# Performance work log

Hardware: AMD Instinct MI355X
Metric: run time of the kernel (lower is better)

The kernel has to match this reference:

```python
import jax, jax.numpy as jnp
import numpy as np

HEADS = 2
HID = 128
IN_DIM = 128
OUT_DIM = 1
N_NODES = 50000
NEG_SLOPE = 0.2  # PyG GATConv default
EPS = 1e-16


def setup_inputs() -> dict:
    key = jax.random.key(0)
    ks = jax.random.split(key, 16)
    N, E = N_NODES, 800000
    x = jax.random.normal(ks[0], (N, IN_DIM), dtype=jnp.float32)
    edge_index = jax.random.randint(ks[1], (2, E), 0, N, dtype=jnp.int32)
    s = 0.1
    # GATConv 1: in=128 -> heads=2, out=128 per head
    W1 = jax.random.normal(ks[2], (IN_DIM, HEADS * HID), dtype=jnp.float32) * s
    a_src1 = jax.random.normal(ks[3], (HEADS, HID), dtype=jnp.float32) * s
    a_dst1 = jax.random.normal(ks[4], (HEADS, HID), dtype=jnp.float32) * s
    b1 = jnp.zeros((HEADS * HID,), dtype=jnp.float32)
    # GATConv 2: in=256 -> heads=2, out=128 per head
    W2 = jax.random.normal(ks[5], (HEADS * HID, HEADS * HID), dtype=jnp.float32) * s
    a_src2 = jax.random.normal(ks[6], (HEADS, HID), dtype=jnp.float32) * s
    a_dst2 = jax.random.normal(ks[7], (HEADS, HID), dtype=jnp.float32) * s
    b2 = jnp.zeros((HEADS * HID,), dtype=jnp.float32)
    # post_mp: Linear(256,128) -> Dropout -> Linear(128,1)
    Wp1 = jax.random.normal(ks[8], (HEADS * HID, HID), dtype=jnp.float32) * s
    bp1 = jnp.zeros((HID,), dtype=jnp.float32)
    Wp2 = jax.random.normal(ks[9], (HID, OUT_DIM), dtype=jnp.float32) * s
    bp2 = jnp.zeros((OUT_DIM,), dtype=jnp.float32)
    return {"x": x, "edge_index": edge_index,
            "W1": W1, "a_src1": a_src1, "a_dst1": a_dst1, "b1": b1,
            "W2": W2, "a_src2": a_src2, "a_dst2": a_dst2, "b2": b2,
            "Wp1": Wp1, "bp1": bp1, "Wp2": Wp2, "bp2": bp2}


def gat_conv(x, src, dst, W, a_src, a_dst, b, num_nodes):
    """PyG-style GATConv (concat=True). src/dst already include self-loops."""
    N = num_nodes
    h = (x @ W).reshape(N, HEADS, HID)                        # [N,H,C]
    alpha_s = jnp.einsum('nhc,hc->nh', h, a_src)              # [N,H]
    alpha_d = jnp.einsum('nhc,hc->nh', h, a_dst)              # [N,H]
    e = jax.nn.leaky_relu(alpha_s[src] + alpha_d[dst], NEG_SLOPE)  # [E,H]
    # segment softmax over destination node
    emax = jax.ops.segment_max(e, dst, num_segments=N)        # [N,H]
    emax = jnp.where(jnp.isfinite(emax), emax, 0.0)
    w = jnp.exp(e - emax[dst])                                # [E,H]
    denom = jax.ops.segment_sum(w, dst, num_segments=N)       # [N,H]
    alpha = w / (denom[dst] + EPS)                            # [E,H]
    out = jax.ops.segment_sum(h[src] * alpha[:, :, None], dst, num_segments=N)
    return out.reshape(N, HEADS * HID) + b


def reference(x, edge_index, W1, a_src1, a_dst1, b1, W2, a_src2, a_dst2, b2,
              Wp1, bp1, Wp2, bp2):
    N = x.shape[0]
    loops = jnp.arange(N, dtype=edge_index.dtype)
    src = jnp.concatenate([edge_index[0], loops])
    dst = jnp.concatenate([edge_index[1], loops])
    h = gat_conv(x, src, dst, W1, a_src1, a_dst1, b1, N)
    h = jax.nn.relu(h)  # dropout is identity in eval mode
    h = gat_conv(h, src, dst, W2, a_src2, a_dst2, b2, N)
    h = jax.nn.relu(h)
    h = h @ Wp1 + bp1
    h = h @ Wp2 + bp2
    return jax.nn.sigmoid(h)
```

## Files before the change

### kernel.cpp

```cpp
#include <hip/hip_runtime.h>

#define HID 128
#define C2 256
#define NEG 0.2f

typedef __bf16 v8bf __attribute__((ext_vector_type(8)));
typedef float  v4f  __attribute__((ext_vector_type(4)));
typedef float  v2f  __attribute__((ext_vector_type(2)));
typedef unsigned short us8 __attribute__((ext_vector_type(8)));

__device__ __forceinline__ float bf2f(unsigned short u) {
    union { float f; unsigned int i; } v; v.i = ((unsigned int)u) << 16; return v.f;
}
__device__ __forceinline__ unsigned short f2bf(float f) {
    union { float f; unsigned int i; } v; v.f = f;
    unsigned int r = v.i + 0x7FFFu + ((v.i >> 16) & 1u);
    return (unsigned short)(r >> 16);
}
__device__ __forceinline__ unsigned char f2fp8(float f) {
    return (unsigned char)(__builtin_amdgcn_cvt_pk_fp8_f32(f, f, 0, false) & 0xFF);
}
__device__ __forceinline__ float lrelu(float x) { return x > 0.f ? x : NEG * x; }

__global__ __launch_bounds__(256) void packB(const float* __restrict__ W,
                                             unsigned short* __restrict__ out,
                                             int K, int N) {
    int idx = blockIdx.x * 256 + threadIdx.x;
    int ksteps = K >> 5;
    int total = (N >> 4) * ksteps * 64;
    if (idx >= total) return;
    int lane = idx & 63;
    int rest = idx >> 6;
    int nt = rest / ksteps, k0 = rest - nt * ksteps;
    int n = nt * 16 + (lane & 15);
    int kb = k0 * 32 + (lane >> 4) * 8;
    us8 v;
#pragma unroll
    for (int j = 0; j < 8; ++j) v[j] = f2bf(W[(size_t)(kb + j) * N + n]);
    *(us8*)(out + (size_t)idx * 8) = v;
}

__global__ void zero_int(int* p, int n) {
    int i = blockIdx.x * 256 + threadIdx.x;
    if (i < n) p[i] = 0;
}

__global__ void hist_rank_kernel(const int* __restrict__ ei, int* __restrict__ cnt,
                                 int* __restrict__ rank, int E) {
    int i = blockIdx.x * 256 + threadIdx.x;
    if (i >= E) return;
    int d = ei[E + i];
    rank[i] = atomicAdd(&cnt[d], 1);
}

__global__ __launch_bounds__(256) void scanA(const int* __restrict__ cnt, int* __restrict__ rs,
                                             int* __restrict__ part, int N) {
    __shared__ int s[256];
    int t = threadIdx.x, i = blockIdx.x * 256 + t;
    int v = (i < N) ? cnt[i] : 0;
    s[t] = v; __syncthreads();
    for (int off = 1; off < 256; off <<= 1) {
        int x = (t >= off) ? s[t - off] : 0;
        __syncthreads();
        s[t] += x;
        __syncthreads();
    }
    if (i < N) rs[i] = s[t] - v;
    if (t == 255) part[blockIdx.x] = s[255];
}

__global__ __launch_bounds__(256) void scanB(int* __restrict__ part, int n) {
    __shared__ int s[256];
    int t = threadIdx.x;
    int v = (t < n) ? part[t] : 0;
    s[t] = v; __syncthreads();
    for (int off = 1; off < 256; off <<= 1) {
        int x = (t >= off) ? s[t - off] : 0;
        __syncthreads();
        s[t] += x;
        __syncthreads();
    }
    if (t < n) part[t] = s[t] - v;
}

__global__ void scanC(int* __restrict__ rs, const int* __restrict__ part, int N, int E) {
    int i = blockIdx.x * 256 + threadIdx.x;
    if (i < N) rs[i] += part[blockIdx.x];
    if (i == 0) rs[N] = E;
}

__global__ void scatter_kernel(const int* __restrict__ ei, const int* __restrict__ rs,
                               const int* __restrict__ rank, int* __restrict__ csr, int E) {
    int i = blockIdx.x * 256 + threadIdx.x;
    if (i >= E) return;
    int s = ei[i], d = ei[E + i];
    csr[rs[d] + rank[i]] = s;
}

template<bool AFP32, int G>
__global__ __launch_bounds__(256) void gemm_alpha(const void* __restrict__ Av,
                                                  const unsigned short* __restrict__ Bp,
                                                  const float* __restrict__ asrc,
                                                  const float* __restrict__ adst,
                                                  float* __restrict__ asd,
                                                  unsigned char* __restrict__ C,
                                                  int M, int N, int K) {
    int ksteps = K >> 5;
    int ngrp = N >> 7;
    int mtiles = M >> 4;
    int groups = (mtiles + G - 1) / G;
    int w = (blockIdx.x << 2) + (threadIdx.x >> 6);
    int mp = w / ngrp, g = w - mp * ngrp;
    if (mp >= groups) return;
    int lane = threadIdx.x & 63;
    int l16 = lane & 15, quad = lane >> 4;

    int mrow[G];
#pragma unroll
    for (int gi = 0; gi < G; ++gi) {
        int mt = mp * G + gi;
        mrow[gi] = (mt < mtiles ? mt : mtiles - 1) * 16 + l16;
    }

    const unsigned short* Bf = Bp + ((size_t)(g * 8) * ksteps << 9) + lane * 8;
    v4f acc[G][8];
#pragma unroll
    for (int gi = 0; gi < G; ++gi)
#pragma unroll
        for (int t = 0; t < 8; ++t) acc[gi][t] = (v4f){0, 0, 0, 0};

    for (int k0 = 0; k0 < ksteps; ++k0) {
        v8bf a[G];
        if (AFP32) {
            const float* A = (const float*)Av;
#pragma unroll
            for (int gi = 0; gi < G; ++gi) {
                const float* p = A + (size_t)mrow[gi] * K + k0 * 32 + quad * 8;
                float4 u0 = *(const float4*)p, u1 = *(const float4*)(p + 4);
                a[gi][0]=(__bf16)u0.x; a[gi][1]=(__bf16)u0.y; a[gi][2]=(__bf16)u0.z; a[gi][3]=(__bf16)u0.w;
                a[gi][4]=(__bf16)u1.x; a[gi][5]=(__bf16)u1.y; a[gi][6]=(__bf16)u1.z; a[gi][7]=(__bf16)u1.w;
            }
        } else {
            const unsigned short* A = (const unsigned short*)Av;
#pragma unroll
            for (int gi = 0; gi < G; ++gi)
                a[gi] = *(const v8bf*)(A + (size_t)mrow[gi] * K + k0 * 32 + quad * 8);
        }
#pragma unroll
        for (int t = 0; t < 8; ++t) {
            v8bf bfr = *(const v8bf*)(Bf + ((size_t)(t * ksteps + k0) << 9));
#pragma unroll
            for (int gi = 0; gi < G; ++gi)
                acc[gi][t] = __builtin_amdgcn_mfma_f32_16x16x32_bf16(a[gi], bfr, acc[gi][t], 0, 0, 0);
        }
    }

    int n0 = g << 7;
    float sv[8], dv[8];
#pragma unroll
    for (int t = 0; t < 8; ++t) {
        int col = n0 + t * 16 + l16;
        sv[t] = asrc[col];
        dv[t] = adst[col];
    }
#pragma unroll
    for (int gi = 0; gi < G; ++gi) {
        int mt = mp * G + gi;
        if (mt >= mtiles) break;
        int row0 = mt * 16 + quad * 4;
#pragma unroll
        for (int r = 0; r < 4; ++r) {
            float sa = 0.f, sd = 0.f;
#pragma unroll
            for (int t = 0; t < 8; ++t) {
                int col = n0 + t * 16 + l16;
                float hv = acc[gi][t][r];
                C[(size_t)(row0 + r) * N + col] = f2fp8(hv);
                sa += hv * sv[t];
                sd += hv * dv[t];
            }
#pragma unroll
            for (int off = 8; off; off >>= 1) {
                sa += __shfl_xor(sa, off);
                sd += __shfl_xor(sd, off);
            }
            if (l16 == 0) {
                int row = row0 + r;
                asd[(size_t)row * 4 + g]     = sa;
                asd[(size_t)row * 4 + 2 + g] = sd;
            }
        }
    }
}

__global__ __launch_bounds__(256) void agg_kernel(const int* __restrict__ rs,
                                                  const int* __restrict__ csr,
                                                  const unsigned char* __restrict__ h,
                                                  const float* __restrict__ asd,
                                                  const float* __restrict__ bias,
                                                  unsigned short* __restrict__ out, int N) {
    int d = blockIdx.x * 4 + (threadIdx.x >> 6);
    if (d >= N) return;
    int lane = threadIdx.x & 63;
    int beg = rs[d], end = rs[d + 1];
    int e2 = lane >> 5;
    int sub = lane & 31;
    int head = sub >> 4;
    float adh = asd[(size_t)d * 4 + 2 + head];
    int cbase = sub * 8;
    const unsigned char* hc = h + cbase;
    float a[8];
#pragma unroll
    for (int j = 0; j < 8; ++j) a[j] = 0.f;
    float den = 0.f;
#pragma unroll 2
    for (int i = beg; i < end; i += 2) {
        int ei = i + e2;
        bool valid = ei < end;
        int s = csr[valid ? ei : end - 1];
        float e = lrelu(asd[(size_t)s * 4 + head] + adh);
        float wgt = valid ? __expf(e) : 0.f;
        den += wgt;
        uint2 u = *(const uint2*)(hc + (size_t)s * C2);
        v2f p0 = __builtin_amdgcn_cvt_pk_f32_fp8(u.x, false);
        v2f p1 = __builtin_amdgcn_cvt_pk_f32_fp8(u.x, true);
        v2f p2 = __builtin_amdgcn_cvt_pk_f32_fp8(u.y, false);
        v2f p3 = __builtin_amdgcn_cvt_pk_f32_fp8(u.y, true);
        a[0] += wgt * p0.x; a[1] += wgt * p0.y;
        a[2] += wgt * p1.x; a[3] += wgt * p1.y;
        a[4] += wgt * p2.x; a[5] += wgt * p2.y;
        a[6] += wgt * p3.x; a[7] += wgt * p3.y;
    }
#pragma unroll
    for (int j = 0; j < 8; ++j) a[j] += __shfl_xor(a[j], 32);
    den += __shfl_xor(den, 32);
    if (e2 == 0) {
        float wS = __expf(lrelu(asd[(size_t)d * 4 + head] + adh));
        uint2 u = *(const uint2*)(hc + (size_t)d * C2);
        v2f p0 = __builtin_amdgcn_cvt_pk_f32_fp8(u.x, false);
        v2f p1 = __builtin_amdgcn_cvt_pk_f32_fp8(u.x, true);
        v2f p2 = __builtin_amdgcn_cvt_pk_f32_fp8(u.y, false);
        v2f p3 = __builtin_amdgcn_cvt_pk_f32_fp8(u.y, true);
        a[0] += wS * p0.x; a[1] += wS * p0.y;
        a[2] += wS * p1.x; a[3] += wS * p1.y;
        a[4] += wS * p2.x; a[5] += wS * p2.y;
        a[6] += wS * p3.x; a[7] += wS * p3.y;
        float rden = 1.f / (den + wS + 1e-16f);
        us8 o;
#pragma unroll
        for (int j = 0; j < 8; ++j) o[j] = f2bf(fmaxf(a[j] * rden + bias[cbase + j], 0.f));
        *(us8*)(out + (size_t)d * C2 + cbase) = o;
    }
}

template<int G>
__global__ __launch_bounds__(256) void gemm_final(const unsigned short* __restrict__ A,
                                                  const unsigned short* __restrict__ Bp,
                                                  const float* __restrict__ bp1,
                                                  const float* __restrict__ wp2,
                                                  const float* __restrict__ bp2,
                                                  float* __restrict__ out,
                                                  int M, int K) {
    int ksteps = K >> 5;
    int mtiles = M >> 4;
    int groups = (mtiles + G - 1) / G;
    int mp = (blockIdx.x << 2) + (threadIdx.x >> 6);
    if (mp >= groups) return;
    int lane = threadIdx.x & 63;
    int l16 = lane & 15, quad = lane >> 4;

    int mrow[G];
#pragma unroll
    for (int gi = 0; gi < G; ++gi) {
        int mt = mp * G + gi;
        mrow[gi] = (mt < mtiles ? mt : mtiles - 1) * 16 + l16;
    }

    const unsigned short* Bf = Bp + lane * 8;
    v4f acc[G][8];
#pragma unroll
    for (int gi = 0; gi < G; ++gi)
#pragma unroll
        for (int t = 0; t < 8; ++t) acc[gi][t] = (v4f){0, 0, 0, 0};
    for (int k0 = 0; k0 < ksteps; ++k0) {
        v8bf a[G];
#pragma unroll
        for (int gi = 0; gi < G; ++gi)
            a[gi] = *(const v8bf*)(A + (size_t)mrow[gi] * K + k0 * 32 + quad * 8);
#pragma unroll
        for (int t = 0; t < 8; ++t) {
            v8bf bfr = *(const v8bf*)(Bf + ((size_t)(t * ksteps + k0) << 9));
#pragma unroll
            for (int gi = 0; gi < G; ++gi)
                acc[gi][t] = __builtin_amdgcn_mfma_f32_16x16x32_bf16(a[gi], bfr, acc[gi][t], 0, 0, 0);
        }
    }
    float wv[8], bv[8];
#pragma unroll
    for (int t = 0; t < 8; ++t) {
        int col = t * 16 + l16;
        wv[t] = wp2[col];
        bv[t] = bp1[col];
    }
    float bias2 = bp2[0];
#pragma unroll
    for (int gi = 0; gi < G; ++gi) {
        int mt = mp * G + gi;
        if (mt >= mtiles) break;
        int row0 = mt * 16 + quad * 4;
#pragma unroll
        for (int r = 0; r < 4; ++r) {
            float s = 0.f;
#pragma unroll
            for (int t = 0; t < 8; ++t) s += (acc[gi][t][r] + bv[t]) * wv[t];
#pragma unroll
            for (int off = 8; off; off >>= 1) s += __shfl_xor(s, off);
            if (l16 == 0) {
                float xv = s + bias2;
                out[row0 + r] = 1.f / (1.f + __expf(-xv));
            }
        }
    }
}

extern "C" void kernel_launch(void* const* d_in, const int* in_sizes, int n_in,
                              void* d_out, int out_size, void* d_ws, size_t ws_size,
                              hipStream_t stream) {
    const float* x   = (const float*)d_in[0];
    const int*   ei  = (const int*)d_in[1];
    const float* W1  = (const float*)d_in[2];
    const float* as1 = (const float*)d_in[3];
    const float* ad1 = (const float*)d_in[4];
    const float* b1  = (const float*)d_in[5];
    const float* W2  = (const float*)d_in[6];
    const float* as2 = (const float*)d_in[7];
    const float* ad2 = (const float*)d_in[8];
    const float* b2  = (const float*)d_in[9];
    const float* Wp1 = (const float*)d_in[10];
    const float* bp1 = (const float*)d_in[11];
    const float* Wp2 = (const float*)d_in[12];
    const float* bp2 = (const float*)d_in[13];
    float* out = (float*)d_out;

    int NN = in_sizes[0] / HID;
    int E  = in_sizes[1] / 2;

    char* ws = (char*)d_ws;
    size_t off = 0;
    auto alloc = [&](size_t bytes) -> char* {
        char* p = ws + off;
        off += (bytes + 255) & ~(size_t)255;
        return p;
    };
    unsigned char*  bufH = (unsigned char*)alloc((size_t)NN * C2);
    unsigned short* bufO = (unsigned short*)alloc((size_t)NN * C2 * 2);
    float* asd = (float*)alloc((size_t)NN * 4 * sizeof(float));
    int* rs    = (int*)alloc((size_t)(NN + 1) * 4);
    int* cnt   = (int*)alloc((size_t)NN * 4);
    int* rank  = (int*)alloc((size_t)E * 4);
    int* csr   = (int*)alloc((size_t)E * 4);
    int* part  = (int*)alloc(1024);
    unsigned short* W1p  = (unsigned short*)alloc((size_t)HID * C2 * 2);
    unsigned short* W2p  = (unsigned short*)alloc((size_t)C2 * C2 * 2);
    unsigned short* Wp1p = (unsigned short*)alloc((size_t)C2 * HID * 2);

    int nchunk = (NN + 255) / 256;
    int eblk   = (E + 255) / 256;

    packB<<<(HID * C2 / 8 + 255) / 256, 256, 0, stream>>>(W1, W1p, HID, C2);
    packB<<<(C2 * C2 / 8 + 255) / 256, 256, 0, stream>>>(W2, W2p, C2, C2);
    packB<<<(C2 * HID / 8 + 255) / 256, 256, 0, stream>>>(Wp1, Wp1p, C2, HID);

    zero_int<<<nchunk, 256, 0, stream>>>(cnt, NN);
    hist_rank_kernel<<<eblk, 256, 0, stream>>>(ei, cnt, rank, E);
    scanA<<<nchunk, 256, 0, stream>>>(cnt, rs, part, NN);
    scanB<<<1, 256, 0, stream>>>(part, nchunk);
    scanC<<<nchunk, 256, 0, stream>>>(rs, part, NN, E);
    scatter_kernel<<<eblk, 256, 0, stream>>>(ei, rs, rank, csr, E);

    const int G = 2;
    int mtiles = NN / 16;
    int groups = (mtiles + G - 1) / G;
    int wgemm = groups * 2;
    int aggGrid = (NN + 3) / 4;

    gemm_alpha<true, G><<<(wgemm + 3) / 4, 256, 0, stream>>>(x, W1p, as1, ad1, asd, bufH, NN, C2, HID);
    agg_kernel<<<aggGrid, 256, 0, stream>>>(rs, csr, bufH, asd, b1, bufO, NN);
    gemm_alpha<false, G><<<(wgemm + 3) / 4, 256, 0, stream>>>(bufO, W2p, as2, ad2, asd, bufH, NN, C2, C2);
    agg_kernel<<<aggGrid, 256, 0, stream>>>(rs, csr, bufH, asd, b2, bufO, NN);
    gemm_final<G><<<(groups + 3) / 4, 256, 0, stream>>>(bufO, Wp1p, bp1, Wp2, bp2, out, NN, C2);
}
```

Measured before the change: 299.0 us.

## Stage B tiles in LDS shared across waves in GEMMs, pack agg FMAs, memset counts

```diff
diff --git a/kernel.cpp b/kernel.cpp
--- a/kernel.cpp
+++ b/kernel.cpp
@@ -40,11 +40,6 @@
     *(us8*)(out + (size_t)idx * 8) = v;
 }
 
-__global__ void zero_int(int* p, int n) {
-    int i = blockIdx.x * 256 + threadIdx.x;
-    if (i < n) p[i] = 0;
-}
-
 __global__ void hist_rank_kernel(const int* __restrict__ ei, int* __restrict__ cnt,
                                  int* __restrict__ rank, int E) {
     int i = blockIdx.x * 256 + threadIdx.x;
@@ -105,53 +100,66 @@
                                                   float* __restrict__ asd,
                                                   unsigned char* __restrict__ C,
                                                   int M, int N, int K) {
+    const int kc = 4;
     int ksteps = K >> 5;
     int ngrp = N >> 7;
     int mtiles = M >> 4;
-    int groups = (mtiles + G - 1) / G;
-    int w = (blockIdx.x << 2) + (threadIdx.x >> 6);
-    int mp = w / ngrp, g = w - mp * ngrp;
-    if (mp >= groups) return;
-    int lane = threadIdx.x & 63;
+    int bm = 4 * G;
+    int g = blockIdx.x % ngrp, mblk = blockIdx.x / ngrp;
+    int wv = threadIdx.x >> 6, lane = threadIdx.x & 63;
     int l16 = lane & 15, quad = lane >> 4;
+    int mt0 = mblk * bm + wv * G;
+
+    __shared__ unsigned short Bs[8 * kc * 512];
 
     int mrow[G];
 #pragma unroll
     for (int gi = 0; gi < G; ++gi) {
-        int mt = mp * G + gi;
+        int mt = mt0 + gi;
         mrow[gi] = (mt < mtiles ? mt : mtiles - 1) * 16 + l16;
     }
 
-    const unsigned short* Bf = Bp + ((size_t)(g * 8) * ksteps << 9) + lane * 8;
+    const us8* srcB = (const us8*)Bp + (size_t)(g * 8) * ksteps * 64;
     v4f acc[G][8];
 #pragma unroll
     for (int gi = 0; gi < G; ++gi)
 #pragma unroll
         for (int t = 0; t < 8; ++t) acc[gi][t] = (v4f){0, 0, 0, 0};
 
-    for (int k0 = 0; k0 < ksteps; ++k0) {
-        v8bf a[G];
-        if (AFP32) {
-            const float* A = (const float*)Av;
-#pragma unroll
-            for (int gi = 0; gi < G; ++gi) {
-                const float* p = A + (size_t)mrow[gi] * K + k0 * 32 + quad * 8;
-                float4 u0 = *(const float4*)p, u1 = *(const float4*)(p + 4);
-                a[gi][0]=(__bf16)u0.x; a[gi][1]=(__bf16)u0.y; a[gi][2]=(__bf16)u0.z; a[gi][3]=(__bf16)u0.w;
-                a[gi][4]=(__bf16)u1.x; a[gi][5]=(__bf16)u1.y; a[gi][6]=(__bf16)u1.z; a[gi][7]=(__bf16)u1.w;
-            }
-        } else {
-            const unsigned short* A = (const unsigned short*)Av;
-#pragma unroll
-            for (int gi = 0; gi < G; ++gi)
-                a[gi] = *(const v8bf*)(A + (size_t)mrow[gi] * K + k0 * 32 + quad * 8);
-        }
-#pragma unroll
-        for (int t = 0; t < 8; ++t) {
-            v8bf bfr = *(const v8bf*)(Bf + ((size_t)(t * ksteps + k0) << 9));
-#pragma unroll
-            for (int gi = 0; gi < G; ++gi)
-                acc[gi][t] = __builtin_amdgcn_mfma_f32_16x16x32_bf16(a[gi], bfr, acc[gi][t], 0, 0, 0);
+    for (int c0 = 0; c0 < ksteps; c0 += kc) {
+        __syncthreads();
+        for (int f = threadIdx.x; f < 8 * kc * 64; f += 256) {
+            int t = f >> 8;
+            int rem = f & 255;
+            int kr = rem >> 6, l = rem & 63;
+            ((us8*)Bs)[f] = srcB[((size_t)t * ksteps + c0 + kr) * 64 + l];
+        }
+        __syncthreads();
+        for (int kr = 0; kr < kc; ++kr) {
+            int k0 = c0 + kr;
+            v8bf a[G];
+            if (AFP32) {
+                const float* A = (const float*)Av;
+#pragma unroll
+                for (int gi = 0; gi < G; ++gi) {
+                    const float* p = A + (size_t)mrow[gi] * K + k0 * 32 + quad * 8;
+                    float4 u0 = *(const float4*)p, u1 = *(const float4*)(p + 4);
+                    a[gi][0]=(__bf16)u0.x; a[gi][1]=(__bf16)u0.y; a[gi][2]=(__bf16)u0.z; a[gi][3]=(__bf16)u0.w;
+                    a[gi][4]=(__bf16)u1.x; a[gi][5]=(__bf16)u1.y; a[gi][6]=(__bf16)u1.z; a[gi][7]=(__bf16)u1.w;
+                }
+            } else {
+                const unsigned short* A = (const unsigned short*)Av;
+#pragma unroll
+                for (int gi = 0; gi < G; ++gi)
+                    a[gi] = *(const v8bf*)(A + (size_t)mrow[gi] * K + k0 * 32 + quad * 8);
+            }
+#pragma unroll
+            for (int t = 0; t < 8; ++t) {
+                v8bf bfr = ((const v8bf*)Bs)[(t * kc + kr) * 64 + lane];
+#pragma unroll
+                for (int gi = 0; gi < G; ++gi)
+                    acc[gi][t] = __builtin_amdgcn_mfma_f32_16x16x32_bf16(a[gi], bfr, acc[gi][t], 0, 0, 0);
+            }
         }
     }
 
@@ -165,7 +173,7 @@
     }
 #pragma unroll
     for (int gi = 0; gi < G; ++gi) {
-        int mt = mp * G + gi;
+        int mt = mt0 + gi;
         if (mt >= mtiles) break;
         int row0 = mt * 16 + quad * 4;
 #pragma unroll
@@ -209,9 +217,7 @@
     float adh = asd[(size_t)d * 4 + 2 + head];
     int cbase = sub * 8;
     const unsigned char* hc = h + cbase;
-    float a[8];
-#pragma unroll
-    for (int j = 0; j < 8; ++j) a[j] = 0.f;
+    v2f a01 = {0, 0}, a23 = {0, 0}, a45 = {0, 0}, a67 = {0, 0};
     float den = 0.f;
 #pragma unroll 2
     for (int i = beg; i < end; i += 2) {
@@ -222,15 +228,13 @@
         float wgt = valid ? __expf(e) : 0.f;
         den += wgt;
         uint2 u = *(const uint2*)(hc + (size_t)s * C2);
-        v2f p0 = __builtin_amdgcn_cvt_pk_f32_fp8(u.x, false);
-        v2f p1 = __builtin_amdgcn_cvt_pk_f32_fp8(u.x, true);
-        v2f p2 = __builtin_amdgcn_cvt_pk_f32_fp8(u.y, false);
-        v2f p3 = __builtin_amdgcn_cvt_pk_f32_fp8(u.y, true);
-        a[0] += wgt * p0.x; a[1] += wgt * p0.y;
-        a[2] += wgt * p1.x; a[3] += wgt * p1.y;
-        a[4] += wgt * p2.x; a[5] += wgt * p2.y;
-        a[6] += wgt * p3.x; a[7] += wgt * p3.y;
-    }
+        v2f w2 = {wgt, wgt};
+        a01 += w2 * __builtin_amdgcn_cvt_pk_f32_fp8(u.x, false);
+        a23 += w2 * __builtin_amdgcn_cvt_pk_f32_fp8(u.x, true);
+        a45 += w2 * __builtin_amdgcn_cvt_pk_f32_fp8(u.y, false);
+        a67 += w2 * __builtin_amdgcn_cvt_pk_f32_fp8(u.y, true);
+    }
+    float a[8] = {a01.x, a01.y, a23.x, a23.y, a45.x, a45.y, a67.x, a67.y};
 #pragma unroll
     for (int j = 0; j < 8; ++j) a[j] += __shfl_xor(a[j], 32);
     den += __shfl_xor(den, 32);
@@ -261,58 +265,73 @@
                                                   const float* __restrict__ bp2,
                                                   float* __restrict__ out,
                                                   int M, int K) {
+    const int kc = 4;
     int ksteps = K >> 5;
     int mtiles = M >> 4;
-    int groups = (mtiles + G - 1) / G;
-    int mp = (blockIdx.x << 2) + (threadIdx.x >> 6);
-    if (mp >= groups) return;
-    int lane = threadIdx.x & 63;
+    int bm = 4 * G;
+    int mblk = blockIdx.x;
+    int wv = threadIdx.x >> 6, lane = threadIdx.x & 63;
     int l16 = lane & 15, quad = lane >> 4;
+    int mt0 = mblk * bm + wv * G;
+
+    __shared__ unsigned short Bs[8 * kc * 512];
 
     int mrow[G];
 #pragma unroll
     for (int gi = 0; gi < G; ++gi) {
-        int mt = mp * G + gi;
+        int mt = mt0 + gi;
         mrow[gi] = (mt < mtiles ? mt : mtiles - 1) * 16 + l16;
     }
 
-    const unsigned short* Bf = Bp + lane * 8;
+    const us8* srcB = (const us8*)Bp;
     v4f acc[G][8];
 #pragma unroll
     for (int gi = 0; gi < G; ++gi)
 #pragma unroll
         for (int t = 0; t < 8; ++t) acc[gi][t] = (v4f){0, 0, 0, 0};
-    for (int k0 = 0; k0 < ksteps; ++k0) {
-        v8bf a[G];
-#pragma unroll
-        for (int gi = 0; gi < G; ++gi)
-            a[gi] = *(const v8bf*)(A + (size_t)mrow[gi] * K + k0 * 32 + quad * 8);
-#pragma unroll
-        for (int t = 0; t < 8; ++t) {
-            v8bf bfr = *(const v8bf*)(Bf + ((size_t)(t * ksteps + k0) << 9));
+
+    for (int c0 = 0; c0 < ksteps; c0 += kc) {
+        __syncthreads();
+        for (int f = threadIdx.x; f < 8 * kc * 64; f += 256) {
+            int t = f >> 8;
+            int rem = f & 255;
+            int kr = rem >> 6, l = rem & 63;
+            ((us8*)Bs)[f] = srcB[((size_t)t * ksteps + c0 + kr) * 64 + l];
+        }
+        __syncthreads();
+        for (int kr = 0; kr < kc; ++kr) {
+            int k0 = c0 + kr;
+            v8bf a[G];
 #pragma unroll
             for (int gi = 0; gi < G; ++gi)
-                acc[gi][t] = __builtin_amdgcn_mfma_f32_16x16x32_bf16(a[gi], bfr, acc[gi][t], 0, 0, 0);
-        }
-    }
-    float wv[8], bv[8];
+                a[gi] = *(const v8bf*)(A + (size_t)mrow[gi] * K + k0 * 32 + quad * 8);
+#pragma unroll
+            for (int t = 0; t < 8; ++t) {
+                v8bf bfr = ((const v8bf*)Bs)[(t * kc + kr) * 64 + lane];
+#pragma unroll
+                for (int gi = 0; gi < G; ++gi)
+                    acc[gi][t] = __builtin_amdgcn_mfma_f32_16x16x32_bf16(a[gi], bfr, acc[gi][t], 0, 0, 0);
+            }
+        }
+    }
+    float wv8[8], bv[8];
 #pragma unroll
     for (int t = 0; t < 8; ++t) {
         int col = t * 16 + l16;
-        wv[t] = wp2[col];
+        wv8[t] = wp2[col];
         bv[t] = bp1[col];
     }
     float bias2 = bp2[0];
 #pragma unroll
     for (int gi = 0; gi < G; ++gi) {
-        int mt = mp * G + gi;
+        int mt = mt0 + gi;
         if (mt >= mtiles) break;
         int row0 = mt * 16 + quad * 4;
 #pragma unroll
         for (int r = 0; r < 4; ++r) {
             float s = 0.f;
 #pragma unroll
-            for (int t = 0; t < 8; ++t) s += (acc[gi][t][r] + bv[t]) * wv[t];
+            for (int t = 0; t < 8; ++t) s += (acc[gi][t][r] + bv[t]) * wv8[t];
 #pragma unroll
             for (int off = 8; off; off >>= 1) s += __shfl_xor(s, off);
             if (l16 == 0) {
@@ -371,7 +390,7 @@
     packB<<<(C2 * C2 / 8 + 255) / 256, 256, 0, stream>>>(W2, W2p, C2, C2);
     packB<<<(C2 * HID / 8 + 255) / 256, 256, 0, stream>>>(Wp1, Wp1p, C2, HID);
 
-    zero_int<<<nchunk, 256, 0, stream>>>(cnt, NN);
+    hipMemsetAsync(cnt, 0, (size_t)NN * 4, stream);
     hist_rank_kernel<<<eblk, 256, 0, stream>>>(ei, cnt, rank, E);
     scanA<<<nchunk, 256, 0, stream>>>(cnt, rs, part, NN);
     scanB<<<1, 256, 0, stream>>>(part, nchunk);
@@ -380,13 +399,13 @@
 
     const int G = 2;
     int mtiles = NN / 16;
-    int groups = (mtiles + G - 1) / G;
-    int wgemm = groups * 2;
+    int bm = 4 * G;
+    int groups = (mtiles + bm - 1) / bm;
     int aggGrid = (NN + 3) / 4;
 
-    gemm_alpha<true, G><<<(wgemm + 3) / 4, 256, 0, stream>>>(x, W1p, as1, ad1, asd, bufH, NN, C2, HID);
+    gemm_alpha<true, G><<<groups * 2, 256, 0, stream>>>(x, W1p, as1, ad1, asd, bufH, NN, C2, HID);
     agg_kernel<<<aggGrid, 256, 0, stream>>>(rs, csr, bufH, asd, b1, bufO, NN);
-    gemm_alpha<false, G><<<(wgemm + 3) / 4, 256, 0, stream>>>(bufO, W2p, as2, ad2, asd, bufH, NN, C2, C2);
+    gemm_alpha<false, G><<<groups * 2, 256, 0, stream>>>(bufO, W2p, as2, ad2, asd, bufH, NN, C2, C2);
     agg_kernel<<<aggGrid, 256, 0, stream>>>(rs, csr, bufH, asd, b2, bufO, NN);
-    gemm_final<G><<<(groups + 3) / 4, 256, 0, stream>>>(bufO, Wp1p, bp1, Wp2, bp2, out, NN, C2);
-}
+    gemm_final<G><<<groups, 256, 0, stream>>>(bufO, Wp1p, bp1, Wp2, bp2, out, NN, C2);
+}
```

New measurement: 302.4 us. Within noise of the previous version (+1.1%).

## Fuse prep kernels, overlap CSR scatter with GEMM, and vectorize fp8 stores

Applied to the files above, without the earlier changes.

```diff
diff --git a/kernel.cpp b/kernel.cpp
--- a/kernel.cpp
+++ b/kernel.cpp
@@ -17,22 +17,18 @@
     unsigned int r = v.i + 0x7FFFu + ((v.i >> 16) & 1u);
     return (unsigned short)(r >> 16);
 }
-__device__ __forceinline__ unsigned char f2fp8(float f) {
-    return (unsigned char)(__builtin_amdgcn_cvt_pk_fp8_f32(f, f, 0, false) & 0xFF);
-}
 __device__ __forceinline__ float lrelu(float x) { return x > 0.f ? x : NEG * x; }
 
-__global__ __launch_bounds__(256) void packB(const float* __restrict__ W,
-                                             unsigned short* __restrict__ out,
-                                             int K, int N) {
-    int idx = blockIdx.x * 256 + threadIdx.x;
+__device__ __forceinline__ void packB_body(const float* __restrict__ W,
+                                           unsigned short* __restrict__ out,
+                                           int K, int N, int idx) {
     int ksteps = K >> 5;
     int total = (N >> 4) * ksteps * 64;
     if (idx >= total) return;
     int lane = idx & 63;
     int rest = idx >> 6;
-    int nt = rest / ksteps, k0 = rest - nt * ksteps;
-    int n = nt * 16 + (lane & 15);
+    int tt = rest / ksteps, k0 = rest - tt * ksteps;
+    int n = (tt >> 3) * 128 + (lane & 15) * 8 + (tt & 7);
     int kb = k0 * 32 + (lane >> 4) * 8;
     us8 v;
 #pragma unroll
@@ -40,14 +36,20 @@
     *(us8*)(out + (size_t)idx * 8) = v;
 }
 
-__global__ void zero_int(int* p, int n) {
-    int i = blockIdx.x * 256 + threadIdx.x;
-    if (i < n) p[i] = 0;
-}
-
-__global__ void hist_rank_kernel(const int* __restrict__ ei, int* __restrict__ cnt,
-                                 int* __restrict__ rank, int E) {
-    int i = blockIdx.x * 256 + threadIdx.x;
+__global__ __launch_bounds__(256) void prep_kernel(const float* __restrict__ W1, unsigned short* W1p,
+                                                   const float* __restrict__ W2, unsigned short* W2p,
+                                                   const float* __restrict__ Wp1, unsigned short* Wp1p,
+                                                   const int* __restrict__ ei, int* __restrict__ cnt,
+                                                   int* __restrict__ rank, int E,
+                                                   int b1, int b2, int b3) {
+    int b = blockIdx.x;
+    if (b < b1) { packB_body(W1, W1p, HID, C2, b * 256 + threadIdx.x); return; }
+    b -= b1;
+    if (b < b2) { packB_body(W2, W2p, C2, C2, b * 256 + threadIdx.x); return; }
+    b -= b2;
+    if (b < b3) { packB_body(Wp1, Wp1p, C2, HID, b * 256 + threadIdx.x); return; }
+    b -= b3;
+    int i = b * 256 + threadIdx.x;
     if (i >= E) return;
     int d = ei[E + i];
     rank[i] = atomicAdd(&cnt[d], 1);
@@ -89,14 +91,6 @@
     if (i == 0) rs[N] = E;
 }
 
-__global__ void scatter_kernel(const int* __restrict__ ei, const int* __restrict__ rs,
-                               const int* __restrict__ rank, int* __restrict__ csr, int E) {
-    int i = blockIdx.x * 256 + threadIdx.x;
-    if (i >= E) return;
-    int s = ei[i], d = ei[E + i];
-    csr[rs[d] + rank[i]] = s;
-}
-
 template<bool AFP32, int G>
 __global__ __launch_bounds__(256) void gemm_alpha(const void* __restrict__ Av,
                                                   const unsigned short* __restrict__ Bp,
@@ -104,21 +98,34 @@
                                                   const float* __restrict__ adst,
                                                   float* __restrict__ asd,
                                                   unsigned char* __restrict__ C,
-                                                  int M, int N, int K) {
+                                                  int M, int N, int K, int gemmBlocks,
+                                                  const int* __restrict__ ei,
+                                                  const int* __restrict__ rs,
+                                                  const int* __restrict__ rank,
+                                                  int* __restrict__ csr, int E) {
+    if (blockIdx.x >= gemmBlocks) {
+        int i = (blockIdx.x - gemmBlocks) * 256 + threadIdx.x;
+        if (i < E) {
+            int s = ei[i], d = ei[E + i];
+            csr[rs[d] + rank[i]] = s;
+        }
+        return;
+    }
     int ksteps = K >> 5;
     int ngrp = N >> 7;
     int mtiles = M >> 4;
+    int w = (blockIdx.x << 2) + (threadIdx.x >> 6);
     int groups = (mtiles + G - 1) / G;
-    int w = (blockIdx.x << 2) + (threadIdx.x >> 6);
     int mp = w / ngrp, g = w - mp * ngrp;
     if (mp >= groups) return;
     int lane = threadIdx.x & 63;
     int l16 = lane & 15, quad = lane >> 4;
+    int mt0 = mp * G;
 
     int mrow[G];
 #pragma unroll
     for (int gi = 0; gi < G; ++gi) {
-        int mt = mp * G + gi;
+        int mt = mt0 + gi;
         mrow[gi] = (mt < mtiles ? mt : mtiles - 1) * 16 + l16;
     }
 
@@ -156,16 +163,16 @@
     }
 
     int n0 = g << 7;
+    int cb = n0 + l16 * 8;
     float sv[8], dv[8];
 #pragma unroll
     for (int t = 0; t < 8; ++t) {
-        int col = n0 + t * 16 + l16;
-        sv[t] = asrc[col];
-        dv[t] = adst[col];
+        sv[t] = asrc[cb + t];
+        dv[t] = adst[cb + t];
     }
 #pragma unroll
     for (int gi = 0; gi < G; ++gi) {
-        int mt = mp * G + gi;
+        int mt = mt0 + gi;
         if (mt >= mtiles) break;
         int row0 = mt * 16 + quad * 4;
 #pragma unroll
@@ -173,12 +180,14 @@
             float sa = 0.f, sd = 0.f;
 #pragma unroll
             for (int t = 0; t < 8; ++t) {
-                int col = n0 + t * 16 + l16;
-                float hv = acc[gi][t][r];
-                C[(size_t)(row0 + r) * N + col] = f2fp8(hv);
-                sa += hv * sv[t];
-                sd += hv * dv[t];
+                sa += acc[gi][t][r] * sv[t];
+                sd += acc[gi][t][r] * dv[t];
             }
+            unsigned int w0 = __builtin_amdgcn_cvt_pk_fp8_f32(acc[gi][0][r], acc[gi][1][r], 0, false);
+            w0 = __builtin_amdgcn_cvt_pk_fp8_f32(acc[gi][2][r], acc[gi][3][r], w0, true);
+            unsigned int w1 = __builtin_amdgcn_cvt_pk_fp8_f32(acc[gi][4][r], acc[gi][5][r], 0, false);
+            w1 = __builtin_amdgcn_cvt_pk_fp8_f32(acc[gi][6][r], acc[gi][7][r], w1, true);
+            *(uint2*)(C + (size_t)(row0 + r) * N + cb) = (uint2){w0, w1};
 #pragma unroll
             for (int off = 8; off; off >>= 1) {
                 sa += __shfl_xor(sa, off);
@@ -209,9 +218,7 @@
     float adh = asd[(size_t)d * 4 + 2 + head];
     int cbase = sub * 8;
     const unsigned char* hc = h + cbase;
-    float a[8];
-#pragma unroll
-    for (int j = 0; j < 8; ++j) a[j] = 0.f;
+    v2f a01 = {0, 0}, a23 = {0, 0}, a45 = {0, 0}, a67 = {0, 0};
     float den = 0.f;
 #pragma unroll 2
     for (int i = beg; i < end; i += 2) {
@@ -222,15 +229,13 @@
         float wgt = valid ? __expf(e) : 0.f;
         den += wgt;
         uint2 u = *(const uint2*)(hc + (size_t)s * C2);
-        v2f p0 = __builtin_amdgcn_cvt_pk_f32_fp8(u.x, false);
-        v2f p1 = __builtin_amdgcn_cvt_pk_f32_fp8(u.x, true);
-        v2f p2 = __builtin_amdgcn_cvt_pk_f32_fp8(u.y, false);
-        v2f p3 = __builtin_amdgcn_cvt_pk_f32_fp8(u.y, true);
-        a[0] += wgt * p0.x; a[1] += wgt * p0.y;
-        a[2] += wgt * p1.x; a[3] += wgt * p1.y;
-        a[4] += wgt * p2.x; a[5] += wgt * p2.y;
-        a[6] += wgt * p3.x; a[7] += wgt * p3.y;
-    }
+        v2f w2 = {wgt, wgt};
+        a01 += w2 * __builtin_amdgcn_cvt_pk_f32_fp8(u.x, false);
+        a23 += w2 * __builtin_amdgcn_cvt_pk_f32_fp8(u.x, true);
+        a45 += w2 * __builtin_amdgcn_cvt_pk_f32_fp8(u.y, false);
+        a67 += w2 * __builtin_amdgcn_cvt_pk_f32_fp8(u.y, true);
+    }
+    float a[8] = {a01.x, a01.y, a23.x, a23.y, a45.x, a45.y, a67.x, a67.y};
 #pragma unroll
     for (int j = 0; j < 8; ++j) a[j] += __shfl_xor(a[j], 32);
     den += __shfl_xor(den, 32);
@@ -295,12 +300,12 @@
                 acc[gi][t] = __builtin_amdgcn_mfma_f32_16x16x32_bf16(a[gi], bfr, acc[gi][t], 0, 0, 0);
         }
     }
-    float wv[8], bv[8];
+    int cb = l16 * 8;
+    float wv8[8], bv[8];
 #pragma unroll
     for (int t = 0; t < 8; ++t) {
-        int col = t * 16 + l16;
-        wv[t] = wp2[col];
-        bv[t] = bp1[col];
+        wv8[t] = wp2[cb + t];
+        bv[t] = bp1[cb + t];
     }
     float bias2 = bp2[0];
 #pragma unroll
@@ -312,7 +317,7 @@
         for (int r = 0; r < 4; ++r) {
             float s = 0.f;
 #pragma unroll
-            for (int t = 0; t < 8; ++t) s += (acc[gi][t][r] + bv[t]) * wv[t];
+            for (int t = 0; t < 8; ++t) s += (acc[gi][t][r] + bv[t]) * wv8[t];
 #pragma unroll
             for (int off = 8; off; off >>= 1) s += __shfl_xor(s, off);
             if (l16 == 0) {
@@ -367,26 +372,29 @@
     int nchunk = (NN + 255) / 256;
     int eblk   = (E + 255) / 256;
 
-    packB<<<(HID * C2 / 8 + 255) / 256, 256, 0, stream>>>(W1, W1p, HID, C2);
-    packB<<<(C2 * C2 / 8 + 255) / 256, 256, 0, stream>>>(W2, W2p, C2, C2);
-    packB<<<(C2 * HID / 8 + 255) / 256, 256, 0, stream>>>(Wp1, Wp1p, C2, HID);
-
-    zero_int<<<nchunk, 256, 0, stream>>>(cnt, NN);
-    hist_rank_kernel<<<eblk, 256, 0, stream>>>(ei, cnt, rank, E);
+    int pb1 = (HID * C2 / 8 + 255) / 256;
+    int pb2 = (C2 * C2 / 8 + 255) / 256;
+    int pb3 = (C2 * HID / 8 + 255) / 256;
+    hipMemsetAsync(cnt, 0, (size_t)NN * 4, stream);
+    prep_kernel<<<pb1 + pb2 + pb3 + eblk, 256, 0, stream>>>(W1, W1p, W2, W2p, Wp1, Wp1p,
+                                                            ei, cnt, rank, E, pb1, pb2, pb3);
     scanA<<<nchunk, 256, 0, stream>>>(cnt, rs, part, NN);
     scanB<<<1, 256, 0, stream>>>(part, nchunk);
     scanC<<<nchunk, 256, 0, stream>>>(rs, part, NN, E);
-    scatter_kernel<<<eblk, 256, 0, stream>>>(ei, rs, rank, csr, E);
 
     const int G = 2;
     int mtiles = NN / 16;
     int groups = (mtiles + G - 1) / G;
-    int wgemm = groups * 2;
+    int gemmBlocks = (groups * 2 + 3) / 4;
     int aggGrid = (NN + 3) / 4;
 
-    gemm_alpha<true, G><<<(wgemm + 3) / 4, 256, 0, stream>>>(x, W1p, as1, ad1, asd, bufH, NN, C2, HID);
+    gemm_alpha<true, G><<<gemmBlocks + eblk, 256, 0, stream>>>(x, W1p, as1, ad1, asd, bufH,
+                                                               NN, C2, HID, gemmBlocks,
+                                                               ei, rs, rank, csr, E);
     agg_kernel<<<aggGrid, 256, 0, stream>>>(rs, csr, bufH, asd, b1, bufO, NN);
-    gemm_alpha<false, G><<<(wgemm + 3) / 4, 256, 0, stream>>>(bufO, W2p, as2, ad2, asd, bufH, NN, C2, C2);
+    gemm_alpha<false, G><<<gemmBlocks, 256, 0, stream>>>(bufO, W2p, as2, ad2, asd, bufH,
+                                                         NN, C2, C2, gemmBlocks,
+                                                         nullptr, nullptr, nullptr, nullptr, 0);
     agg_kernel<<<aggGrid, 256, 0, stream>>>(rs, csr, bufH, asd, b2, bufO, NN);
     gemm_final<G><<<(groups + 3) / 4, 256, 0, stream>>>(bufO, Wp1p, bp1, Wp2, bp2, out, NN, C2);
 }
```

New measurement: 287.8 us. 1.04x faster.
